# Kernel tuning notes

Measured on AMD Instinct MI355X. Metric: run time of the kernel, lower is better.

Reference implementation:

```python
import jax, jax.numpy as jnp
import numpy as np

EPS = 1e-12  # torch F.normalize eps
K = 32       # num_clusters (hardcoded in module)

def l2norm(v, axis):
    n = jnp.sqrt(jnp.sum(v * v, axis=axis, keepdims=True))
    return v / jnp.maximum(n, EPS)

def setup_inputs() -> dict:
    key = jax.random.key(0)
    k1, k2, k3, k4 = jax.random.split(key, 4)
    B, M, D = 64, 128, 2048
    x = jax.random.normal(k1, (B, M, D), dtype=jnp.float32)
    # ragged lengths in [1, M]
    lengths = jax.random.randint(k2, (B,), 0, M, dtype=jnp.int32) + 1
    init_sc = 1.0 / np.sqrt(D)
    W = init_sc * jax.random.normal(k3, (K, D), dtype=jnp.float32)  # fc1.weight
    C = init_sc * jax.random.normal(k4, (K, D), dtype=jnp.float32)  # centroids
    return {"x": x, "lengths": lengths, "W": W, "C": C}

def reference(x, lengths, W, C):
    # x: [B,M,D] padded frames, lengths: [B] valid frame counts
    B, M, D = x.shape
    mask = (jnp.arange(M)[None, :] < lengths[:, None]).astype(x.dtype)  # [B,M]
    cnt = lengths.astype(x.dtype)[:, None]                              # [B,1]
    # avg pooling over valid (raw, un-normalized) frames
    avgpool = jnp.sum(x * mask[:, :, None], axis=1) / cnt               # [B,D]
    # per-frame L2 normalize
    xn = l2norm(x, axis=-1)                                             # [B,M,D]
    # soft assignment: linear (no bias) + softmax over clusters
    logits = jnp.einsum('bmd,kd->bmk', xn, W)
    a = jax.nn.softmax(logits, axis=-1) * mask[:, :, None]              # [B,M,K]
    # VLAD residual aggregation, GEMM form:
    # sum_m a[b,m,k]*(xn[b,m,:] - C[k,:]) = (a^T xn) - C * sum_m a
    ax = jnp.einsum('bmk,bmd->bkd', a, xn)                              # [B,K,D]
    asum = jnp.sum(a, axis=1)                                           # [B,K]
    vlad = ax - asum[:, :, None] * C[None, :, :]                        # [B,K,D]
    # intra-normalize per cluster, flatten, global L2 normalize
    vlad = l2norm(vlad, axis=2)
    vlad = vlad.reshape(B, K * D)
    vlad = l2norm(vlad, axis=1)
    return jnp.concatenate([avgpool, vlad], axis=1)                     # [B, D + K*D]
```

## Files before the change

kernel.cpp:

```cpp
#include <hip/hip_runtime.h>
#include <math.h>

#define BB 64
#define MM 128
#define DDIM 2048
#define KK 32
#define NFR (BB*MM)
#define OUTROW (DDIM + KK*DDIM)

typedef __attribute__((ext_vector_type(8))) short bf16x8;
typedef __attribute__((ext_vector_type(4))) float f32x4;

__device__ __forceinline__ short f2bf(float f) {
  unsigned u = __builtin_bit_cast(unsigned, f);
  u += 0x7fffu + ((u >> 16) & 1u);
  return (short)(u >> 16);
}
__device__ __forceinline__ unsigned pack2(float lo, float hi) {
  return (unsigned)(unsigned short)f2bf(lo) | ((unsigned)(unsigned short)f2bf(hi) << 16);
}

__global__ __launch_bounds__(256) void k_prep(const float* __restrict__ W,
                                              short* __restrict__ Wb) {
  int i = (blockIdx.x * 256 + threadIdx.x) * 8;
  float4 a = *(const float4*)(W + i);
  float4 b = *(const float4*)(W + i + 4);
  bf16x8 o = {f2bf(a.x), f2bf(a.y), f2bf(a.z), f2bf(a.w),
              f2bf(b.x), f2bf(b.y), f2bf(b.z), f2bf(b.w)};
  *(bf16x8*)(Wb + i) = o;
}

__global__ __launch_bounds__(256, 2) void k_logits(const float* __restrict__ x,
    const int* __restrict__ lengths, const short* __restrict__ Wb,
    short* __restrict__ aT, float* __restrict__ asum_p) {
  const int t = threadIdx.x, wv = t >> 6, lane = t & 63;
  const int l15 = lane & 15, quad = lane >> 4;
  const int fg = blockIdx.x;
  const int g0 = fg * 16;
  const int b  = fg >> 3;
  const int m0 = (fg & 7) * 16;
  const int len = lengths[b];
  const bool av = (m0 + l15) < len;

  const float* xrow = x + (size_t)(g0 + l15) * DDIM + wv * 512 + quad * 8;
  const short* w0   = Wb + l15 * DDIM + wv * 512 + quad * 8;
  const short* w1   = w0 + 16 * DDIM;

  f32x4 c0 = {0.f, 0.f, 0.f, 0.f}, c1 = {0.f, 0.f, 0.f, 0.f};
  float ssq = 0.f;
  #pragma unroll
  for (int h = 0; h < 2; ++h) {
    float4 xa[8], xc[8];
    bf16x8 B0[8], B1[8];
    #pragma unroll
    for (int s = 0; s < 8; ++s) {
      const int so = h * 8 + s;
      if (av) {
        xa[s] = *(const float4*)(xrow + so * 32);
        xc[s] = *(const float4*)(xrow + so * 32 + 4);
      } else {
        xa[s] = make_float4(0.f, 0.f, 0.f, 0.f);
        xc[s] = make_float4(0.f, 0.f, 0.f, 0.f);
      }
      B0[s] = *(const bf16x8*)(w0 + so * 32);
      B1[s] = *(const bf16x8*)(w1 + so * 32);
    }
    #pragma unroll
    for (int s = 0; s < 8; ++s) {
      ssq = fmaf(xa[s].x, xa[s].x, ssq); ssq = fmaf(xa[s].y, xa[s].y, ssq);
      ssq = fmaf(xa[s].z, xa[s].z, ssq); ssq = fmaf(xa[s].w, xa[s].w, ssq);
      ssq = fmaf(xc[s].x, xc[s].x, ssq); ssq = fmaf(xc[s].y, xc[s].y, ssq);
      ssq = fmaf(xc[s].z, xc[s].z, ssq); ssq = fmaf(xc[s].w, xc[s].w, ssq);
      bf16x8 A = {f2bf(xa[s].x), f2bf(xa[s].y), f2bf(xa[s].z), f2bf(xa[s].w),
                  f2bf(xc[s].x), f2bf(xc[s].y), f2bf(xc[s].z), f2bf(xc[s].w)};
      c0 = __builtin_amdgcn_mfma_f32_16x16x32_bf16(A, B0[s], c0, 0, 0, 0);
      c1 = __builtin_amdgcn_mfma_f32_16x16x32_bf16(A, B1[s], c1, 0, 0, 0);
    }
  }

  ssq += __shfl_xor(ssq, 16, 64);
  ssq += __shfl_xor(ssq, 32, 64);
  __shared__ float sq[4][16];
  __shared__ float lg[4][16][33];
  if (quad == 0) sq[wv][l15] = ssq;
  #pragma unroll
  for (int r = 0; r < 4; ++r) {
    lg[wv][quad * 4 + r][l15]      = c0[r];
    lg[wv][quad * 4 + r][16 + l15] = c1[r];
  }
  __syncthreads();

  const int fr = t >> 4, kk = (t & 15) * 2;
  float s0 = 0.f, s1 = 0.f;
  #pragma unroll
  for (int w = 0; w < 4; ++w) { s0 += lg[w][fr][kk]; s1 += lg[w][fr][kk + 1]; }
  float ss  = sq[0][fr] + sq[1][fr] + sq[2][fr] + sq[3][fr];
  float inv = 1.f / fmaxf(sqrtf(ss), 1e-12f);
  s0 *= inv; s1 *= inv;
  float mx = fmaxf(s0, s1);
  mx = fmaxf(mx, __shfl_xor(mx, 1, 64));
  mx = fmaxf(mx, __shfl_xor(mx, 2, 64));
  mx = fmaxf(mx, __shfl_xor(mx, 4, 64));
  mx = fmaxf(mx, __shfl_xor(mx, 8, 64));
  float e0 = __expf(s0 - mx), e1 = __expf(s1 - mx);
  float se = e0 + e1;
  se += __shfl_xor(se, 1, 64);
  se += __shfl_xor(se, 2, 64);
  se += __shfl_xor(se, 4, 64);
  se += __shfl_xor(se, 8, 64);
  const bool valid = (m0 + fr) < len;
  float rr = valid ? (1.f / se) : 0.f;
  float a0 = e0 * rr, a1 = e1 * rr;

  __syncthreads();
  lg[0][fr][kk] = a0; lg[0][fr][kk + 1] = a1;
  __syncthreads();
  if (t < KK) {
    float s = 0.f;
    #pragma unroll
    for (int f = 0; f < 16; ++f) s += lg[0][f][t];
    asum_p[(size_t)fg * KK + t] = s;
  }
  short* ap = aT + (size_t)b * KK * MM + m0 + fr;
  ap[(size_t)kk * MM]       = f2bf(a0 * inv);
  ap[(size_t)(kk + 1) * MM] = f2bf(a1 * inv);
}

__global__ __launch_bounds__(256, 2) void k_vlad(const float* __restrict__ x,
    const int* __restrict__ lengths, const float* __restrict__ Cc,
    const short* __restrict__ aT, const float* __restrict__ asum_p,
    float* __restrict__ out, float* __restrict__ ssq_part) {
  const int t = threadIdx.x, wv = t >> 6, lane = t & 63;
  const int l15 = lane & 15, quad = lane >> 4;
  const int dc = blockIdx.x, b = blockIdx.y;
  const int dw0 = dc * 256 + wv * 64;
  const int len = lengths[b];

  __shared__ short xbt[4][64][40];
  __shared__ float asl[KK];
  __shared__ float ssw[4][33];

  if (t < KK) {
    float s = 0.f;
    #pragma unroll
    for (int p = 0; p < 8; ++p) s += asum_p[(size_t)(b * 8 + p) * KK + t];
    asl[t] = s;
  }

  const float* xb  = x  + (size_t)b * MM * DDIM;
  const short* at0 = aT + (size_t)b * KK * MM + l15 * MM + quad * 8;

  const int q4   = l15 * 4;
  const int mrow = quad * 2;
  const int keyw = l15 & 3;
  const int keyr = (l15 >> 2) & 3;

  bf16x8 A0[4], A1[4];
  #pragma unroll
  for (int ms = 0; ms < 4; ++ms) {
    A0[ms] = *(const bf16x8*)(at0 + ms * 32);
    A1[ms] = *(const bf16x8*)(at0 + 16 * MM + ms * 32);
  }

  float4 v0[16], v1[16];
  #pragma unroll
  for (int ms = 0; ms < 4; ++ms) {
    #pragma unroll
    for (int p = 0; p < 4; ++p) {
      const int m = ms * 32 + p * 8 + mrow;
      const float* xr = xb + (size_t)m * DDIM + dw0 + q4;
      v0[ms * 4 + p] = (m < len) ? *(const float4*)xr
                                 : make_float4(0.f, 0.f, 0.f, 0.f);
      v1[ms * 4 + p] = (m + 1 < len) ? *(const float4*)(xr + DDIM)
                                     : make_float4(0.f, 0.f, 0.f, 0.f);
    }
  }

  float avg[4] = {0.f, 0.f, 0.f, 0.f};
  #pragma unroll
  for (int i = 0; i < 16; ++i) {
    avg[0] += v0[i].x + v1[i].x;
    avg[1] += v0[i].y + v1[i].y;
    avg[2] += v0[i].z + v1[i].z;
    avg[3] += v0[i].w + v1[i].w;
  }

  f32x4 acc[2][4];
  #pragma unroll
  for (int kt = 0; kt < 2; ++kt)
    #pragma unroll
    for (int nt = 0; nt < 4; ++nt) acc[kt][nt] = (f32x4){0.f, 0.f, 0.f, 0.f};

  #pragma unroll
  for (int ms = 0; ms < 4; ++ms) {
    #pragma unroll
    for (int p = 0; p < 4; ++p) {
      const int i = ms * 4 + p;
      const int mls = (p ^ keyw) * 8 + mrow;
      *(unsigned*)&xbt[wv][q4 + 0][mls] = pack2(v0[i].x, v1[i].x);
      *(unsigned*)&xbt[wv][q4 + 1][mls] = pack2(v0[i].y, v1[i].y);
      *(unsigned*)&xbt[wv][q4 + 2][mls] = pack2(v0[i].z, v1[i].z);
      *(unsigned*)&xbt[wv][q4 + 3][mls] = pack2(v0[i].w, v1[i].w);
    }
    #pragma unroll
    for (int nt = 0; nt < 4; ++nt) {
      bf16x8 B = *(const bf16x8*)&xbt[wv][nt * 16 + l15][(quad ^ keyr) * 8];
      acc[0][nt] = __builtin_amdgcn_mfma_f32_16x16x32_bf16(A0[ms], B, acc[0][nt], 0, 0, 0);
      acc[1][nt] = __builtin_amdgcn_mfma_f32_16x16x32_bf16(A1[ms], B, acc[1][nt], 0, 0, 0);
    }
  }

  #pragma unroll
  for (int c = 0; c < 4; ++c) {
    avg[c] += __shfl_xor(avg[c], 16, 64);
    avg[c] += __shfl_xor(avg[c], 32, 64);
  }
  if (quad == 0) {
    float rl = 1.f / (float)len;
    *(float4*)(out + (size_t)b * OUTROW + dw0 + q4) =
        make_float4(avg[0] * rl, avg[1] * rl, avg[2] * rl, avg[3] * rl);
  }

  __syncthreads();
  float* orow = out + (size_t)b * OUTROW + DDIM;
  #pragma unroll
  for (int kt = 0; kt < 2; ++kt) {
    #pragma unroll
    for (int r = 0; r < 4; ++r) {
      const int k = kt * 16 + quad * 4 + r;
      const float as = asl[k];
      float sqv = 0.f;
      #pragma unroll
      for (int nt = 0; nt < 4; ++nt) {
        const int d = dw0 + nt * 16 + l15;
        float v = acc[kt][nt][r] - as * Cc[(size_t)k * DDIM + d];
        orow[(size_t)k * DDIM + d] = v;
        sqv = fmaf(v, v, sqv);
      }
      sqv += __shfl_xor(sqv, 1, 64);
      sqv += __shfl_xor(sqv, 2, 64);
      sqv += __shfl_xor(sqv, 4, 64);
      sqv += __shfl_xor(sqv, 8, 64);
      if (l15 == 0) ssw[wv][k] = sqv;
    }
  }
  __syncthreads();
  if (t < KK)
    ssq_part[((size_t)dc * BB + b) * KK + t] =
        ssw[0][t] + ssw[1][t] + ssw[2][t] + ssw[3][t];
}

__global__ __launch_bounds__(256) void k_norm(const float* __restrict__ ssq_part,
    float* __restrict__ out) {
  const int t = threadIdx.x;
  const int k = blockIdx.x;
  const int b = blockIdx.y;
  __shared__ float ssk[32];
  if (t < 32) {
    float sk = 0.f;
    #pragma unroll
    for (int dc = 0; dc < 8; ++dc)
      sk += ssq_part[((size_t)dc * BB + b) * KK + t];
    ssk[t] = sk;
  }
  __syncthreads();
  float gss = 0.f, iv_own = 0.f;
  #pragma unroll
  for (int kk = 0; kk < 32; ++kk) {
    float nk = sqrtf(ssk[kk]);
    float iv = 1.f / fmaxf(nk, 1e-12f);
    float nn = nk * iv;
    gss += nn * nn;
    if (kk == k) iv_own = iv;
  }
  float sc = iv_own / fmaxf(sqrtf(gss), 1e-12f);
  float* row = out + (size_t)b * OUTROW + DDIM + (size_t)k * DDIM;
  #pragma unroll
  for (int h = 0; h < 2; ++h) {
    float4* p = (float4*)(row + h * 1024 + t * 4);
    float4 v = *p;
    v.x *= sc; v.y *= sc; v.z *= sc; v.w *= sc;
    *p = v;
  }
}

extern "C" void kernel_launch(void* const* d_in, const int* in_sizes, int n_in,
                              void* d_out, int out_size, void* d_ws, size_t ws_size,
                              hipStream_t stream) {
  const float* x       = (const float*)d_in[0];
  const int*   lengths = (const int*)d_in[1];
  const float* W       = (const float*)d_in[2];
  const float* C       = (const float*)d_in[3];
  float* out = (float*)d_out;

  short* Wb     = (short*)d_ws;
  short* aT     = Wb + (size_t)KK * DDIM;
  float* asum_p = (float*)(aT + (size_t)BB * KK * MM);
  float* ssqp   = asum_p + (size_t)512 * KK;

  k_prep  <<<dim3(32),     256, 0, stream>>>(W, Wb);
  k_logits<<<dim3(512),    256, 0, stream>>>(x, lengths, Wb, aT, asum_p);
  k_vlad  <<<dim3(8, BB),  256, 0, stream>>>(x, lengths, C, aT, asum_p, out, ssqp);
  k_norm  <<<dim3(KK, BB), 256, 0, stream>>>(ssqp, out);
}
```

Measured before the change: 145.9 us.

## Stream x loads per m-slice, stage VLAD output in LDS for coalesced stores

```diff
diff --git a/kernel.cpp b/kernel.cpp
--- a/kernel.cpp
+++ b/kernel.cpp
@@ -126,7 +126,7 @@
   ap[(size_t)(kk + 1) * MM] = f2bf(a1 * inv);
 }
 
-__global__ __launch_bounds__(256, 2) void k_vlad(const float* __restrict__ x,
+__global__ __launch_bounds__(256, 3) void k_vlad(const float* __restrict__ x,
     const int* __restrict__ lengths, const float* __restrict__ Cc,
     const short* __restrict__ aT, const float* __restrict__ asum_p,
     float* __restrict__ out, float* __restrict__ ssq_part) {
@@ -137,8 +137,9 @@
   const int len = lengths[b];
 
   __shared__ short xbt[4][64][40];
+  __shared__ float vst[16][268];
   __shared__ float asl[KK];
-  __shared__ float ssw[4][33];
+  __shared__ float ss32[KK];
 
   if (t < KK) {
     float s = 0.f;
@@ -148,7 +149,7 @@
   }
 
   const float* xb  = x  + (size_t)b * MM * DDIM;
-  const short* at0 = aT + (size_t)b * KK * MM + l15 * MM + quad * 8;
+  const short* at0 = aT + (size_t)b * KK * MM + (size_t)l15 * MM + quad * 8;
 
   const int q4   = l15 * 4;
   const int mrow = quad * 2;
@@ -162,45 +163,35 @@
     A1[ms] = *(const bf16x8*)(at0 + 16 * MM + ms * 32);
   }
 
-  float4 v0[16], v1[16];
+  f32x4 acc[2][4];
+  #pragma unroll
+  for (int kt = 0; kt < 2; ++kt)
+    #pragma unroll
+    for (int nt = 0; nt < 4; ++nt) acc[kt][nt] = (f32x4){0.f, 0.f, 0.f, 0.f};
+  float avg[4] = {0.f, 0.f, 0.f, 0.f};
+
   #pragma unroll
   for (int ms = 0; ms < 4; ++ms) {
+    float4 v0[4], v1[4];
     #pragma unroll
     for (int p = 0; p < 4; ++p) {
       const int m = ms * 32 + p * 8 + mrow;
       const float* xr = xb + (size_t)m * DDIM + dw0 + q4;
-      v0[ms * 4 + p] = (m < len) ? *(const float4*)xr
-                                 : make_float4(0.f, 0.f, 0.f, 0.f);
-      v1[ms * 4 + p] = (m + 1 < len) ? *(const float4*)(xr + DDIM)
-                                     : make_float4(0.f, 0.f, 0.f, 0.f);
-    }
-  }
-
-  float avg[4] = {0.f, 0.f, 0.f, 0.f};
-  #pragma unroll
-  for (int i = 0; i < 16; ++i) {
-    avg[0] += v0[i].x + v1[i].x;
-    avg[1] += v0[i].y + v1[i].y;
-    avg[2] += v0[i].z + v1[i].z;
-    avg[3] += v0[i].w + v1[i].w;
-  }
-
-  f32x4 acc[2][4];
-  #pragma unroll
-  for (int kt = 0; kt < 2; ++kt)
-    #pragma unroll
-    for (int nt = 0; nt < 4; ++nt) acc[kt][nt] = (f32x4){0.f, 0.f, 0.f, 0.f};
-
-  #pragma unroll
-  for (int ms = 0; ms < 4; ++ms) {
+      v0[p] = (m < len) ? *(const float4*)xr : make_float4(0.f, 0.f, 0.f, 0.f);
+      v1[p] = (m + 1 < len) ? *(const float4*)(xr + DDIM)
+                            : make_float4(0.f, 0.f, 0.f, 0.f);
+    }
     #pragma unroll
     for (int p = 0; p < 4; ++p) {
-      const int i = ms * 4 + p;
+      avg[0] += v0[p].x + v1[p].x;
+      avg[1] += v0[p].y + v1[p].y;
+      avg[2] += v0[p].z + v1[p].z;
+      avg[3] += v0[p].w + v1[p].w;
       const int mls = (p ^ keyw) * 8 + mrow;
-      *(unsigned*)&xbt[wv][q4 + 0][mls] = pack2(v0[i].x, v1[i].x);
-      *(unsigned*)&xbt[wv][q4 + 1][mls] = pack2(v0[i].y, v1[i].y);
-      *(unsigned*)&xbt[wv][q4 + 2][mls] = pack2(v0[i].z, v1[i].z);
-      *(unsigned*)&xbt[wv][q4 + 3][mls] = pack2(v0[i].w, v1[i].w);
+      *(unsigned*)&xbt[wv][q4 + 0][mls] = pack2(v0[p].x, v1[p].x);
+      *(unsigned*)&xbt[wv][q4 + 1][mls] = pack2(v0[p].y, v1[p].y);
+      *(unsigned*)&xbt[wv][q4 + 2][mls] = pack2(v0[p].z, v1[p].z);
+      *(unsigned*)&xbt[wv][q4 + 3][mls] = pack2(v0[p].w, v1[p].w);
     }
     #pragma unroll
     for (int nt = 0; nt < 4; ++nt) {
@@ -227,27 +218,36 @@
   for (int kt = 0; kt < 2; ++kt) {
     #pragma unroll
     for (int r = 0; r < 4; ++r) {
-      const int k = kt * 16 + quad * 4 + r;
+      const int kl = quad * 4 + r;
+      const int k  = kt * 16 + kl;
       const float as = asl[k];
-      float sqv = 0.f;
       #pragma unroll
       for (int nt = 0; nt < 4; ++nt) {
         const int d = dw0 + nt * 16 + l15;
-        float v = acc[kt][nt][r] - as * Cc[(size_t)k * DDIM + d];
-        orow[(size_t)k * DDIM + d] = v;
-        sqv = fmaf(v, v, sqv);
+        vst[kl][wv * 64 + nt * 16 + l15] =
+            acc[kt][nt][r] - as * Cc[(size_t)k * DDIM + d];
       }
+    }
+    __syncthreads();
+    #pragma unroll
+    for (int it = 0; it < 4; ++it) {
+      const int kl = it * 4 + wv;
+      const int k  = kt * 16 + kl;
+      float4 v = *(const float4*)&vst[kl][lane * 4];
+      *(float4*)(orow + (size_t)k * DDIM + dc * 256 + lane * 4) = v;
+      float sqv = fmaf(v.x, v.x, fmaf(v.y, v.y, fmaf(v.z, v.z, v.w * v.w)));
       sqv += __shfl_xor(sqv, 1, 64);
       sqv += __shfl_xor(sqv, 2, 64);
       sqv += __shfl_xor(sqv, 4, 64);
       sqv += __shfl_xor(sqv, 8, 64);
-      if (l15 == 0) ssw[wv][k] = sqv;
-    }
-  }
-  __syncthreads();
+      sqv += __shfl_xor(sqv, 16, 64);
+      sqv += __shfl_xor(sqv, 32, 64);
+      if (lane == 0) ss32[k] = sqv;
+    }
+    __syncthreads();
+  }
   if (t < KK)
-    ssq_part[((size_t)dc * BB + b) * KK + t] =
-        ssw[0][t] + ssw[1][t] + ssw[2][t] + ssw[3][t];
+    ssq_part[((size_t)dc * BB + b) * KK + t] = ss32[t];
 }
 
 __global__ __launch_bounds__(256) void k_norm(const float* __restrict__ ssq_part,
```

Result: slower. 148.9 us (+2.0%).
